# Kernel tuning notes

Hardware: AMD Instinct MI355X
Metric: run time of the kernel (lower is better)

Reference implementation:

```python
import jax, jax.numpy as jnp
import numpy as np

B, N_PER, P_PER = 64, 64, 2016   # graphs, nodes/graph, pairs/graph (C(64,2))
IN_DIM, HID, OUT = 64, 128, 10
EDGE_P = 0.125


def _build_graph_structures():
    """Integer preprocessing replicating build_2sets_from_embeddings's
    combinatorics (pairs, iso_type source, triangle-based 2-set edges)."""
    rng = np.random.default_rng(0)
    n, b = N_PER, B
    A = rng.random((b, n, n)) < EDGE_P
    A = np.triu(A, 1)
    A = A | A.transpose(0, 2, 1)                      # symmetric, no self loops
    gs, us, vs = np.nonzero(A)                        # directed edges, both dirs
    edge_index = np.stack([gs * n + us, gs * n + vs]).astype(np.int64)
    batch = np.repeat(np.arange(b), n).astype(np.int64)
    iu, iv = np.triu_indices(n, 1)                    # local pair (u<v) lists
    pidx = np.full((n, n), -1, np.int64)
    pidx[iu, iv] = np.arange(P_PER)
    pidx[iv, iu] = np.arange(P_PER)                   # symmetric lookup = sorted()
    pair_u = (np.arange(b)[:, None] * n + iu[None, :]).ravel().astype(np.int64)
    pair_v = (np.arange(b)[:, None] * n + iv[None, :]).ravel().astype(np.int64)
    iso_type = A[:, iu, iv].astype(np.float32).ravel()[:, None]  # [B*P_PER,1]
    # 2-set edges: pair (u,v) -> sorted(v,w) and sorted(u,w) for every common
    # neighbor w of u and v (matches _build_2set_edges exactly)
    common = A[:, iu, :] & A[:, iv, :]                # (B, P_PER, n)
    g2, ps, ws = np.nonzero(common)
    u, v = iu[ps], iv[ps]
    d1 = pidx[v, ws]
    d2 = pidx[u, ws]
    src = np.concatenate([g2 * P_PER + ps, g2 * P_PER + ps])
    dst = np.concatenate([g2 * P_PER + d1, g2 * P_PER + d2])
    two_edges = np.stack([src, dst]).astype(np.int64)
    two_batch = np.repeat(np.arange(b), P_PER).astype(np.int64)
    return edge_index, batch, pair_u, pair_v, iso_type, two_edges, two_batch


def setup_inputs() -> dict:
    ei, batch, pu, pv, iso, te, tb = _build_graph_structures()
    key = jax.random.key(0)
    ks = jax.random.split(key, 16)
    w = lambda k, i, o: jax.random.normal(k, (i, o), jnp.float32) / np.float32(np.sqrt(i))
    two_in = 2 * HID + 1
    return {
        "x": jax.random.normal(ks[0], (B * N_PER, IN_DIM), jnp.float32),
        "g1_W1_0": w(ks[1], IN_DIM, HID), "g1_W2_0": w(ks[2], IN_DIM, HID),
        "g1_W1_1": w(ks[3], HID, HID),    "g1_W2_1": w(ks[4], HID, HID),
        "g1_W1_2": w(ks[5], HID, HID),    "g1_W2_2": w(ks[6], HID, HID),
        "k_W1_0": w(ks[7], two_in, HID),  "k_W2_0": w(ks[8], two_in, HID),
        "k_W1_1": w(ks[9], HID, HID),     "k_W2_1": w(ks[10], HID, HID),
        "c_W0": w(ks[11], 2 * HID, HID),  "c_b0": jnp.zeros((HID,), jnp.float32),
        "c_W1": w(ks[12], HID, OUT),      "c_b1": jnp.zeros((OUT,), jnp.float32),
        "iso_type": jnp.asarray(iso),
        "edge_index": jnp.asarray(ei), "batch": jnp.asarray(batch),
        "pair_u": jnp.asarray(pu), "pair_v": jnp.asarray(pv),
        "two_edges": jnp.asarray(te), "two_batch": jnp.asarray(tb),
    }


def _mp_layer(h, ei, W1, W2):
    # relu( h @ W1 + scatter_add_{dst}( h[src] @ W2 ) )  -- OneGNNLayer / KSetLayer
    msg = h[ei[0]] @ W2
    agg = jax.ops.segment_sum(msg, ei[1], num_segments=h.shape[0])
    return jax.nn.relu(h @ W1 + agg)


def reference(x, g1_W1_0, g1_W2_0, g1_W1_1, g1_W2_1, g1_W1_2, g1_W2_2,
              k_W1_0, k_W2_0, k_W1_1, k_W2_1,
              c_W0, c_b0, c_W1, c_b1,
              iso_type, edge_index, batch, pair_u, pair_v, two_edges, two_batch):
    h = _mp_layer(x, edge_index, g1_W1_0, g1_W2_0)
    h = _mp_layer(h, edge_index, g1_W1_1, g1_W2_1)
    h = _mp_layer(h, edge_index, g1_W1_2, g1_W2_2)
    graph_emb_1 = jax.ops.segment_sum(h, batch, num_segments=B)
    # 2-set features: [h_u, h_v, iso_type]  -> [P, 2H+1]
    two_x = jnp.concatenate([h[pair_u], h[pair_v], iso_type], axis=1)
    h2 = _mp_layer(two_x, two_edges, k_W1_0, k_W2_0)
    h2 = _mp_layer(h2, two_edges, k_W1_1, k_W2_1)
    graph_emb_2 = jax.ops.segment_sum(h2, two_batch, num_segments=B)
    combined = jnp.concatenate([graph_emb_1, graph_emb_2], axis=1)
    hc = jax.nn.relu(combined @ c_W0 + c_b0)   # Dropout(p=0.5) inactive in eval
    return hc @ c_W1 + c_b1
```

## Files before the change

kernel.cpp:

```cpp
#include <hip/hip_runtime.h>
#include <hip/hip_bf16.h>


typedef short s16x8 __attribute__((ext_vector_type(8)));
typedef float f32x4 __attribute__((ext_vector_type(4)));

__device__ __forceinline__ unsigned short f2bf(float f) {
  union { float f; unsigned u; } x; x.f = f;
  unsigned r = (x.u + 0x7fffu + ((x.u >> 16) & 1u)) >> 16;
  return (unsigned short)r;
}
__device__ __forceinline__ float bf2f(unsigned short h) {
  union { unsigned u; float f; } x; x.u = ((unsigned)h) << 16;
  return x.f;
}
__device__ __forceinline__ float4 ldbf4(const unsigned short* p) {
  ushort4 q = *(const ushort4*)p;
  return make_float4(bf2f(q.x), bf2f(q.y), bf2f(q.z), bf2f(q.w));
}
__device__ __forceinline__ void stbf4(unsigned short* p, float4 v) {
  ushort4 q;
  q.x = f2bf(v.x); q.y = f2bf(v.y); q.z = f2bf(v.z); q.w = f2bf(v.w);
  *(ushort4*)p = q;
}
__device__ __forceinline__ float4 ld4(const float* p) { return *(const float4*)p; }

template<int KCS, int ASTR>
__device__ __forceinline__ void mfma_dual_lds(
    const unsigned short* A, const unsigned short* Wfrag,
    f32x4 (&accA)[8], f32x4 (&accB)[8])
{
  const int lane = threadIdx.x & 63;
  const int wv = threadIdx.x >> 6;
  const int row = wv * 16 + (lane & 15);
  const int k0 = (lane >> 4) << 3;
  const unsigned short* ap = A + row * ASTR + k0;
  const unsigned short* wp = Wfrag + (size_t)lane * 8;
#pragma unroll
  for (int i = 0; i < 8; ++i) { accA[i] = (f32x4)0.f; accB[i] = (f32x4)0.f; }
#pragma unroll
  for (int kc = 0; kc < KCS; ++kc) {
    s16x8 af = *(const s16x8*)(ap + kc * 32);
#pragma unroll
    for (int nt = 0; nt < 8; ++nt) {
      s16x8 b0 = *(const s16x8*)(wp + ((size_t)((nt)*KCS + kc) << 9));
      s16x8 b1 = *(const s16x8*)(wp + ((size_t)((8 + nt) * KCS + kc) << 9));
      accA[nt] = __builtin_amdgcn_mfma_f32_16x16x32_bf16(af, b0, accA[nt], 0, 0, 0);
      accB[nt] = __builtin_amdgcn_mfma_f32_16x16x32_bf16(af, b1, accB[nt], 0, 0, 0);
    }
  }
}

template<int KCS, int ASTR>
__device__ __forceinline__ void mfma_dual_lds16(
    const unsigned short* A, const unsigned short* Wfrag,
    f32x4 (&accA)[2], f32x4 (&accB)[2])
{
  const int lane = threadIdx.x & 63;
  const int w16 = threadIdx.x >> 6;
  const int rw = w16 & 3, ch = w16 >> 2;
  const int row = rw * 16 + (lane & 15);
  const int k0 = (lane >> 4) << 3;
  const unsigned short* ap = A + row * ASTR + k0;
  const unsigned short* wp = Wfrag + (size_t)lane * 8;
  accA[0] = (f32x4)0.f; accA[1] = (f32x4)0.f;
  accB[0] = (f32x4)0.f; accB[1] = (f32x4)0.f;
  __builtin_amdgcn_s_setprio(1);
#pragma unroll
  for (int kc = 0; kc < KCS; ++kc) {
    s16x8 af = *(const s16x8*)(ap + kc * 32);
#pragma unroll
    for (int n2 = 0; n2 < 2; ++n2) {
      int nt = ch * 2 + n2;
      s16x8 b0 = *(const s16x8*)(wp + ((size_t)(nt * KCS + kc) << 9));
      s16x8 b1 = *(const s16x8*)(wp + ((size_t)((8 + nt) * KCS + kc) << 9));
      accA[n2] = __builtin_amdgcn_mfma_f32_16x16x32_bf16(af, b0, accA[n2], 0, 0, 0);
      accB[n2] = __builtin_amdgcn_mfma_f32_16x16x32_bf16(af, b1, accB[n2], 0, 0, 0);
    }
  }
  __builtin_amdgcn_s_setprio(0);
}

__device__ __forceinline__ void epi_lds16(const f32x4 (&accA)[2], const f32x4 (&accB)[2],
    unsigned short (*preS)[136], unsigned short (*msgS)[136])
{
  const int lane = threadIdx.x & 63;
  const int w16 = threadIdx.x >> 6;
  const int rw = w16 & 3, ch = w16 >> 2;
  const int col = lane & 15;
  const int r0 = rw * 16 + ((lane >> 4) << 2);
  __syncthreads();
#pragma unroll
  for (int n2 = 0; n2 < 2; ++n2) {
    int nt = ch * 2 + n2;
#pragma unroll
    for (int r = 0; r < 4; ++r) {
      preS[r0 + r][nt * 16 + col] = f2bf(accA[n2][r]);
      msgS[r0 + r][nt * 16 + col] = f2bf(accB[n2][r]);
    }
  }
  __syncthreads();
}

__device__ __forceinline__ void epi_global(const f32x4 (&accA)[8], const f32x4 (&accB)[8],
    unsigned short (*sOut)[136], unsigned short* Ca, unsigned short* Cb, long tile)
{
  const int tid = threadIdx.x;
  const int lane = tid & 63;
  const int wv = tid >> 6;
  const int col = lane & 15;
  const int r0 = wv * 16 + ((lane >> 4) << 2);
  const long rowBase = tile * 64;
#pragma unroll
  for (int sel = 0; sel < 2; ++sel) {
    __syncthreads();
#pragma unroll
    for (int nt = 0; nt < 8; ++nt) {
#pragma unroll
      for (int r = 0; r < 4; ++r)
        sOut[r0 + r][nt * 16 + col] = f2bf(sel ? accB[nt][r] : accA[nt][r]);
    }
    __syncthreads();
    unsigned short* C = sel ? Cb : Ca;
#pragma unroll
    for (int i = 0; i < 4; ++i) {
      int fi = tid + i * 256;
      int row = fi >> 4;
      int c8 = fi & 15;
      *(uint4*)(C + (rowBase + row) * 128 + c8 * 8) = *(uint4*)&sOut[row][c8 * 8];
    }
  }
}

struct NArgs {
  const float* x;
  const int* ei;
  const int* gstart;
  const unsigned short *Wf0, *Wf1, *Wf2;
  unsigned short* Hn;
  float* ge1;
  int E1;
};

__global__ __launch_bounds__(1024) void node_stage(NArgs a)
{
  __shared__ __align__(16) unsigned short hS[64][136];
  __shared__ __align__(16) unsigned short preS[64][136];
  __shared__ __align__(16) unsigned short msgS[64][136];
  __shared__ int ldeg[64], lcur[64], loff[65];
  __shared__ unsigned short ledge[1024];
  __shared__ float sge[128];

  const int b = blockIdx.x;
  const int t = threadIdx.x;
  const int base = b * 64;

  const int es = a.gstart[b], ee = a.gstart[b + 1];
  if (t < 64) ldeg[t] = 0;
  if (t < 128) sge[t] = 0.f;
  __syncthreads();
  for (int i = es + t; i < ee; i += 1024)
    atomicAdd(&ldeg[a.ei[a.E1 + i] - base], 1);
  __syncthreads();
  if (t < 64) {
    int v = ldeg[t], s = v;
#pragma unroll
    for (int d = 1; d < 64; d <<= 1) {
      int o = __shfl_up(s, d, 64);
      if (t >= d) s += o;
    }
    loff[t] = s - v;
    lcur[t] = s - v;
    if (t == 63) loff[64] = s;
  }
  unsigned short* xs = &preS[0][0];
  for (int i = t; i < 64 * 64; i += 1024) {
    int r = i >> 6, c = i & 63;
    xs[r * 72 + c] = f2bf(a.x[(size_t)(base + r) * 64 + c]);
  }
  __syncthreads();
  for (int i = es + t; i < ee; i += 1024) {
    int s = a.ei[i] - base, d = a.ei[a.E1 + i] - base;
    int pos = atomicAdd(&lcur[d], 1);
    ledge[pos] = (unsigned short)s;
  }
  __syncthreads();

  f32x4 accA[2], accB[2];
  const int grp = t >> 5, f = (t & 31) * 4;

  mfma_dual_lds16<2, 72>(xs, a.Wf0, accA, accB);
  epi_lds16(accA, accB, preS, msgS);
  for (int r = grp; r < 64; r += 32) {
    float4 acc = ldbf4(&preS[r][f]);
    int j1 = loff[r + 1];
    for (int j = loff[r]; j < j1; ++j) {
      float4 m = ldbf4(&msgS[ledge[j]][f]);
      acc.x += m.x; acc.y += m.y; acc.z += m.z; acc.w += m.w;
    }
    stbf4(&hS[r][f], make_float4(fmaxf(acc.x, 0.f), fmaxf(acc.y, 0.f),
                                 fmaxf(acc.z, 0.f), fmaxf(acc.w, 0.f)));
  }
  __syncthreads();

  mfma_dual_lds16<4, 136>(&hS[0][0], a.Wf1, accA, accB);
  epi_lds16(accA, accB, preS, msgS);
  for (int r = grp; r < 64; r += 32) {
    float4 acc = ldbf4(&preS[r][f]);
    int j1 = loff[r + 1];
    for (int j = loff[r]; j < j1; ++j) {
      float4 m = ldbf4(&msgS[ledge[j]][f]);
      acc.x += m.x; acc.y += m.y; acc.z += m.z; acc.w += m.w;
    }
    stbf4(&hS[r][f], make_float4(fmaxf(acc.x, 0.f), fmaxf(acc.y, 0.f),
                                 fmaxf(acc.z, 0.f), fmaxf(acc.w, 0.f)));
  }
  __syncthreads();

  mfma_dual_lds16<4, 136>(&hS[0][0], a.Wf2, accA, accB);
  epi_lds16(accA, accB, preS, msgS);
  {
    float4 g = make_float4(0.f, 0.f, 0.f, 0.f);
    for (int r = grp; r < 64; r += 32) {
      float4 acc = ldbf4(&preS[r][f]);
      int j1 = loff[r + 1];
      for (int j = loff[r]; j < j1; ++j) {
        float4 m = ldbf4(&msgS[ledge[j]][f]);
        acc.x += m.x; acc.y += m.y; acc.z += m.z; acc.w += m.w;
      }
      float4 o = make_float4(fmaxf(acc.x, 0.f), fmaxf(acc.y, 0.f),
                             fmaxf(acc.z, 0.f), fmaxf(acc.w, 0.f));
      stbf4(&hS[r][f], o);
      g.x += o.x; g.y += o.y; g.z += o.z; g.w += o.w;
    }
    atomicAdd(&sge[f + 0], g.x);
    atomicAdd(&sge[f + 1], g.y);
    atomicAdd(&sge[f + 2], g.z);
    atomicAdd(&sge[f + 3], g.w);
  }
  __syncthreads();
  if (t < 128) a.ge1[b * 128 + t] = sge[t];
  {
    int row = t >> 4, c8 = t & 15;
    *(uint4*)(a.Hn + (size_t)(base + row) * 128 + c8 * 8) = *(uint4*)&hS[row][c8 * 8];
  }
}

__global__ __launch_bounds__(256) void hv_gemm(
    const unsigned short* __restrict__ Hn,
    const unsigned short* __restrict__ Wf3, const unsigned short* __restrict__ Wf4,
    unsigned short* __restrict__ HU1, unsigned short* __restrict__ HU2,
    unsigned short* __restrict__ HV1, unsigned short* __restrict__ HV2)
{
  __shared__ __align__(16) unsigned short hS[64][136];
  const int g = blockIdx.x >> 1;
  const int sel = blockIdx.x & 1;
  const int tid = threadIdx.x;
  const unsigned short* src = Hn + (size_t)g * 64 * 128;
#pragma unroll
  for (int i = 0; i < 4; ++i) {
    int fi = tid + i * 256;
    int row = fi >> 4, c8 = fi & 15;
    *(uint4*)&hS[row][c8 * 8] = *(const uint4*)(src + row * 128 + c8 * 8);
  }
  __syncthreads();
  f32x4 accA[8], accB[8];
  mfma_dual_lds<4, 136>(&hS[0][0], sel ? Wf4 : Wf3, accA, accB);
  epi_global(accA, accB, hS, sel ? HV1 : HU1, sel ? HV2 : HU2, g);
}

struct PrepArgs {
  const float* wa[6];
  const float* wb[6];
  unsigned short* Wf[6];
  const int* te; int E2;
  int* degP;
  const int* ei; int E1;
  int* gstart;
  int nCnt;
};

__global__ void prep(PrepArgs p)
{
  int bb = blockIdx.x, t = threadIdx.x;
  if (bb < 88) {
    int gid = bb * 256 + t;
    if (gid < 22528) {
      int pi, local, kcs, kclog;
      if (gid < 2048) { pi = 0; local = gid; kcs = 2; kclog = 1; }
      else { int r = gid - 2048; pi = 1 + (r >> 12); local = r & 4095; kcs = 4; kclog = 2; }
      int lane = local & 63;
      int t1 = local >> 6;
      int kc = t1 & (kcs - 1);
      int t2 = t1 >> kclog;
      int nt = t2 & 7;
      int wsel = t2 >> 3;
      const float* W = wsel ? p.wb[pi] : p.wa[pi];
      int k0 = kc * 32 + ((lane >> 4) << 3);
      int n = nt * 16 + (lane & 15);
      unsigned short tmp[8];
#pragma unroll
      for (int j = 0; j < 8; ++j) tmp[j] = f2bf(W[(size_t)(k0 + j) * 128 + n]);
      *(uint4*)(p.Wf[pi] + (size_t)local * 8) = *(uint4*)tmp;
    }
  } else if (bb < 88 + p.nCnt) {
    int e = (bb - 88) * 256 + t;
    if (e < p.E2) atomicAdd(&p.degP[p.te[p.E2 + e]], 1);
  } else {
    int e = (bb - 88 - p.nCnt) * 256 + t;
    if (e <= p.E1) {
      int ge = (e < p.E1) ? (p.ei[e] >> 6) : 64;
      int gp = (e > 0) ? (p.ei[e - 1] >> 6) : -1;
      for (int g = gp + 1; g <= ge; ++g) p.gstart[g] = e;
    }
  }
}

__global__ __launch_bounds__(256) void scan_reduce(const int* __restrict__ deg,
                                                   int* __restrict__ bsum, int n)
{
  __shared__ int s[256];
  int b = blockIdx.x, t = threadIdx.x;
  int base = b * 1024;
  int v = 0;
#pragma unroll
  for (int i = 0; i < 4; ++i) {
    int idx = base + t + i * 256;
    if (idx < n) v += deg[idx];
  }
  s[t] = v;
  __syncthreads();
  for (int d = 128; d > 0; d >>= 1) {
    if (t < d) s[t] += s[t + d];
    __syncthreads();
  }
  if (t == 0) bsum[b] = s[0];
}

__global__ __launch_bounds__(256) void scan_final(const int* __restrict__ deg,
                                                  const int* __restrict__ bsum,
                                                  int* __restrict__ off,
                                                  int* __restrict__ cur, int n, int nb)
{
  __shared__ int s[256];
  __shared__ int basePfx;
  int b = blockIdx.x, t = threadIdx.x;
  if (t == 0) {
    int acc = 0;
    for (int k = 0; k < b; ++k) acc += bsum[k];
    basePfx = acc;
  }
  int base = b * 1024 + t * 4;
  int v0 = 0, v1 = 0, v2 = 0, v3 = 0;
  if (base + 0 < n) v0 = deg[base + 0];
  if (base + 1 < n) v1 = deg[base + 1];
  if (base + 2 < n) v2 = deg[base + 2];
  if (base + 3 < n) v3 = deg[base + 3];
  s[t] = v0 + v1 + v2 + v3;
  __syncthreads();
  for (int d = 1; d < 256; d <<= 1) {
    int v = (t >= d) ? s[t - d] : 0;
    __syncthreads();
    s[t] += v;
    __syncthreads();
  }
  int run = basePfx + ((t == 0) ? 0 : s[t - 1]);
  if (base + 0 < n) { off[base + 0] = run; cur[base + 0] = run; run += v0; }
  if (base + 1 < n) { off[base + 1] = run; cur[base + 1] = run; run += v1; }
  if (base + 2 < n) { off[base + 2] = run; cur[base + 2] = run; run += v2; }
  if (base + 3 < n) { off[base + 3] = run; cur[base + 3] = run; run += v3; }
  if (b == nb - 1 && t == 0) off[n] = basePfx + bsum[b];
}

__global__ void csr_fill_pair(const int* __restrict__ te, int E2,
                              const int* __restrict__ pu, const int* __restrict__ pv,
                              const float* __restrict__ iso,
                              int* __restrict__ curP, int4* __restrict__ recP)
{
  int e = blockIdx.x * 256 + threadIdx.x;
  if (e >= E2) return;
  int s = te[e], d = te[E2 + e];
  int pos = atomicAdd(&curP[d], 1);
  recP[pos] = make_int4(pu[s], pv[s], __float_as_int(iso[s]), s);
}

__global__ __launch_bounds__(256) void gather_two0_bf(
    const unsigned short* __restrict__ HU1, const unsigned short* __restrict__ HV1,
    const unsigned short* __restrict__ HU2, const unsigned short* __restrict__ HV2,
    const float* __restrict__ iso,
    const float* __restrict__ w1iso, const float* __restrict__ w2iso,
    const int* __restrict__ pu, const int* __restrict__ pv,
    const int* __restrict__ off, const int4* __restrict__ rec,
    unsigned short* __restrict__ out, int P)
{
  int blk = (int)blockIdx.x;
  const int nB = (int)gridDim.x;
  if ((nB & 7) == 0)
    blk = (blk & 7) * (nB >> 3) + (blk >> 3);
  int p = blk * 8 + (threadIdx.x >> 5);
  if (p >= P) return;
  int f = (threadIdx.x & 31) * 4;
  float4 wi1 = ld4(w1iso + f);
  float4 wi2 = ld4(w2iso + f);
  int u0 = pu[p], v0 = pv[p];
  float is0 = iso[p];
  float4 a = ldbf4(HU1 + (size_t)u0 * 128 + f);
  float4 b = ldbf4(HV1 + (size_t)v0 * 128 + f);
  float4 acc;
  acc.x = a.x + b.x + is0 * wi1.x;
  acc.y = a.y + b.y + is0 * wi1.y;
  acc.z = a.z + b.z + is0 * wi1.z;
  acc.w = a.w + b.w + is0 * wi1.w;
  int j = off[p], e1 = off[p + 1];
  for (; j + 1 < e1; j += 2) {
    int4 r0 = rec[j], r1 = rec[j + 1];
    float4 mu0 = ldbf4(HU2 + (size_t)r0.x * 128 + f);
    float4 mv0 = ldbf4(HV2 + (size_t)r0.y * 128 + f);
    float4 mu1 = ldbf4(HU2 + (size_t)r1.x * 128 + f);
    float4 mv1 = ldbf4(HV2 + (size_t)r1.y * 128 + f);
    float i0 = __int_as_float(r0.z), i1 = __int_as_float(r1.z);
    acc.x += mu0.x + mv0.x + i0 * wi2.x + mu1.x + mv1.x + i1 * wi2.x;
    acc.y += mu0.y + mv0.y + i0 * wi2.y + mu1.y + mv1.y + i1 * wi2.y;
    acc.z += mu0.z + mv0.z + i0 * wi2.z + mu1.z + mv1.z + i1 * wi2.z;
    acc.w += mu0.w + mv0.w + i0 * wi2.w + mu1.w + mv1.w + i1 * wi2.w;
  }
  if (j < e1) {
    int4 r0 = rec[j];
    float4 mu0 = ldbf4(HU2 + (size_t)r0.x * 128 + f);
    float4 mv0 = ldbf4(HV2 + (size_t)r0.y * 128 + f);
    float i0 = __int_as_float(r0.z);
    acc.x += mu0.x + mv0.x + i0 * wi2.x;
    acc.y += mu0.y + mv0.y + i0 * wi2.y;
    acc.z += mu0.z + mv0.z + i0 * wi2.z;
    acc.w += mu0.w + mv0.w + i0 * wi2.w;
  }
  stbf4(out + (size_t)p * 128 + f,
        make_float4(fmaxf(acc.x, 0.f), fmaxf(acc.y, 0.f),
                    fmaxf(acc.z, 0.f), fmaxf(acc.w, 0.f)));
}

__global__ __launch_bounds__(64) void pair_l1(
    const unsigned short* __restrict__ H2,
    const unsigned short* __restrict__ Wfrag,
    const int* __restrict__ off, const int4* __restrict__ rec,
    float* __restrict__ gep)
{
  __shared__ __align__(16) unsigned short hS[16][136];
  __shared__ int offS[17];
  __shared__ int recwS[256];
  __shared__ float sge[128];

  const int tid = threadIdx.x;
  int qt = (int)blockIdx.x;
  const int nB = (int)gridDim.x;
  if ((nB & 7) == 0)
    qt = (qt & 7) * (nB >> 3) + (qt >> 3);
  const int r0 = qt * 16;

  if (tid < 17) offS[tid] = off[r0 + tid];
  sge[tid] = 0.f;
  sge[tid + 64] = 0.f;

  {
    const unsigned short* src = H2 + (size_t)r0 * 128;
#pragma unroll
    for (int i = 0; i < 4; ++i) {
      int fi = tid + i * 64;
      int row = fi >> 4, c8 = fi & 15;
      *(uint4*)&hS[row][c8 * 8] = *(const uint4*)(src + row * 128 + c8 * 8);
    }
  }
  __syncthreads();

  const int e0 = offS[0];
  const int ecnt = offS[16] - e0;
  const bool useS = (ecnt <= 256);
  if (useS)
    for (int j = tid; j < ecnt; j += 64) recwS[j] = rec[e0 + j].w;

  const int lane = tid;
  const int arow = lane & 15;
  const int k0 = (lane >> 4) << 3;
  const unsigned short* hp = &hS[0][0] + arow * 136 + k0;
  const unsigned short* wp = Wfrag + (size_t)lane * 8;
  f32x4 acc[8];
#pragma unroll
  for (int nt = 0; nt < 8; ++nt) acc[nt] = (f32x4)0.f;
  __builtin_amdgcn_s_setprio(1);
#pragma unroll
  for (int kc = 0; kc < 4; ++kc) {
    s16x8 ah = *(const s16x8*)(hp + kc * 32);
#pragma unroll
    for (int nt = 0; nt < 8; ++nt) {
      s16x8 b0 = *(const s16x8*)(wp + ((size_t)(nt * 4 + kc) << 9));
      acc[nt] = __builtin_amdgcn_mfma_f32_16x16x32_bf16(ah, b0, acc[nt], 0, 0, 0);
    }
  }
  __builtin_amdgcn_s_setprio(0);
  __syncthreads();

  {
    const int grp = tid >> 5, f = (tid & 31) * 4;
    for (int i = grp; i < 16; i += 2) {
      float4 a = make_float4(0.f, 0.f, 0.f, 0.f);
      int j = offS[i], e1 = offS[i + 1];
      for (; j + 1 < e1; j += 2) {
        int s0 = useS ? recwS[j - e0] : rec[j].w;
        int s1 = useS ? recwS[j + 1 - e0] : rec[j + 1].w;
        float4 m0 = ldbf4(H2 + (size_t)s0 * 128 + f);
        float4 m1 = ldbf4(H2 + (size_t)s1 * 128 + f);
        a.x += m0.x + m1.x; a.y += m0.y + m1.y;
        a.z += m0.z + m1.z; a.w += m0.w + m1.w;
      }
      if (j < e1) {
        int s0 = useS ? recwS[j - e0] : rec[j].w;
        float4 m0 = ldbf4(H2 + (size_t)s0 * 128 + f);
        a.x += m0.x; a.y += m0.y; a.z += m0.z; a.w += m0.w;
      }
      stbf4(&hS[i][f], a);
    }
  }
  __syncthreads();

  __builtin_amdgcn_s_setprio(1);
#pragma unroll
  for (int kc = 0; kc < 4; ++kc) {
    s16x8 ag = *(const s16x8*)(hp + kc * 32);
#pragma unroll
    for (int nt = 0; nt < 8; ++nt) {
      s16x8 b1 = *(const s16x8*)(wp + ((size_t)((8 + nt) * 4 + kc) << 9));
      acc[nt] = __builtin_amdgcn_mfma_f32_16x16x32_bf16(ag, b1, acc[nt], 0, 0, 0);
    }
  }
  __builtin_amdgcn_s_setprio(0);

  const int col0 = lane & 15;
#pragma unroll
  for (int nt = 0; nt < 8; ++nt) {
    float s = fmaxf(acc[nt][0], 0.f) + fmaxf(acc[nt][1], 0.f)
            + fmaxf(acc[nt][2], 0.f) + fmaxf(acc[nt][3], 0.f);
    atomicAdd(&sge[nt * 16 + col0], s);
  }
  __syncthreads();
  gep[(size_t)qt * 128 + tid] = sge[tid];
  gep[(size_t)qt * 128 + tid + 64] = sge[tid + 64];
}

__global__ void classifier(const float* __restrict__ ge1, const float* __restrict__ gep,
                           const float* __restrict__ W0, const float* __restrict__ b0,
                           const float* __restrict__ W1, const float* __restrict__ b1,
                           float* __restrict__ out)
{
  __shared__ float comb[256];
  __shared__ float hc[128];
  int g = blockIdx.x, t = threadIdx.x;
  comb[t] = ge1[g * 128 + t];
  float s2 = 0.f;
  const float* gpr = gep + (size_t)g * 126 * 128 + t;
  for (int i = 0; i < 126; ++i) s2 += gpr[i * 128];
  comb[t + 128] = s2;
  __syncthreads();
  float s = b0[t];
  for (int k = 0; k < 256; ++k) s += comb[k] * W0[k * 128 + t];
  hc[t] = fmaxf(s, 0.f);
  __syncthreads();
  if (t < 10) {
    float s2o = b1[t];
    for (int k = 0; k < 128; ++k) s2o += hc[k] * W1[k * 10 + t];
    out[g * 10 + t] = s2o;
  }
}

extern "C" void kernel_launch(void* const* d_in, const int* in_sizes, int n_in,
                              void* d_out, int out_size, void* d_ws, size_t ws_size,
                              hipStream_t stream)
{
  (void)n_in; (void)out_size; (void)ws_size;
  const float* x       = (const float*)d_in[0];
  const float* g1_W1_0 = (const float*)d_in[1];
  const float* g1_W2_0 = (const float*)d_in[2];
  const float* g1_W1_1 = (const float*)d_in[3];
  const float* g1_W2_1 = (const float*)d_in[4];
  const float* g1_W1_2 = (const float*)d_in[5];
  const float* g1_W2_2 = (const float*)d_in[6];
  const float* k_W1_0  = (const float*)d_in[7];
  const float* k_W2_0  = (const float*)d_in[8];
  const float* k_W1_1  = (const float*)d_in[9];
  const float* k_W2_1  = (const float*)d_in[10];
  const float* c_W0    = (const float*)d_in[11];
  const float* c_b0    = (const float*)d_in[12];
  const float* c_W1    = (const float*)d_in[13];
  const float* c_b1    = (const float*)d_in[14];
  const float* iso     = (const float*)d_in[15];
  const int*   ei      = (const int*)d_in[16];
  const int*   pu      = (const int*)d_in[18];
  const int*   pv      = (const int*)d_in[19];
  const int*   te      = (const int*)d_in[20];

  const int N  = in_sizes[0] / 64;
  const int E1 = in_sizes[16] / 2;
  const int P  = in_sizes[18];
  const int E2 = in_sizes[20] / 2;
  const int B  = 64;
  const int nTiles = P / 64;

  const size_t NH = (size_t)N * 128;
  const size_t PH = (size_t)P * 128;

  float* ge1 = (float*)d_ws;
  float* gep = ge1 + 8192;
  unsigned short* HU1 = (unsigned short*)(gep + (size_t)4 * nTiles * 128);
  unsigned short* HV1 = HU1 + NH;
  unsigned short* HU2 = HV1 + NH;
  unsigned short* HV2 = HU2 + NH;
  unsigned short* H2   = HV2 + NH;
  unsigned short* Hn   = H2 + PH;
  unsigned short* Wf0  = Hn + NH;
  unsigned short* Wf1  = Wf0 + 16384;
  unsigned short* Wf2  = Wf1 + 32768;
  unsigned short* Wf3  = Wf2 + 32768;
  unsigned short* Wf4  = Wf3 + 32768;
  unsigned short* Wf5  = Wf4 + 32768;

  size_t ipOff = ((size_t)((char*)(Wf5 + 32768) - (char*)d_ws) + 15) & ~(size_t)15;
  int4* recP   = (int4*)((char*)d_ws + ipOff);
  int* degP    = (int*)(recP + E2);
  int* offP    = degP + P;
  int* curP    = offP + P + 1;
  int* bsumP   = curP + P;
  int* gstartN = bsumP + 128;

  const int nbP  = (P + 1023) / 1024;
  const int nCnt = (E2 + 255) / 256;
  const int nBnd = (E1 + 256) / 256;

  hipMemsetAsync(degP, 0, (size_t)P * 4, stream);

  PrepArgs pa;
  pa.wa[0] = g1_W1_0;           pa.wb[0] = g1_W2_0;
  pa.wa[1] = g1_W1_1;           pa.wb[1] = g1_W2_1;
  pa.wa[2] = g1_W1_2;           pa.wb[2] = g1_W2_2;
  pa.wa[3] = k_W1_0;            pa.wb[3] = k_W2_0;
  pa.wa[4] = k_W1_0 + 128*128;  pa.wb[4] = k_W2_0 + 128*128;
  pa.wa[5] = k_W1_1;            pa.wb[5] = k_W2_1;
  pa.Wf[0] = Wf0; pa.Wf[1] = Wf1; pa.Wf[2] = Wf2;
  pa.Wf[3] = Wf3; pa.Wf[4] = Wf4; pa.Wf[5] = Wf5;
  pa.te = te; pa.E2 = E2; pa.degP = degP;
  pa.ei = ei; pa.E1 = E1; pa.gstart = gstartN; pa.nCnt = nCnt;
  prep<<<88 + nCnt + nBnd, 256, 0, stream>>>(pa);

  scan_reduce<<<nbP, 256, 0, stream>>>(degP, bsumP, P);
  scan_final<<<nbP, 256, 0, stream>>>(degP, bsumP, offP, curP, P, nbP);
  csr_fill_pair<<<nCnt, 256, 0, stream>>>(te, E2, pu, pv, iso, curP, recP);

  NArgs na;
  na.x = x; na.ei = ei; na.gstart = gstartN; na.E1 = E1;
  na.Wf0 = Wf0; na.Wf1 = Wf1; na.Wf2 = Wf2;
  na.Hn = Hn; na.ge1 = ge1;
  node_stage<<<B, 1024, 0, stream>>>(na);

  hv_gemm<<<2 * B, 256, 0, stream>>>(Hn, Wf3, Wf4, HU1, HU2, HV1, HV2);

  gather_two0_bf<<<(P + 7) / 8, 256, 0, stream>>>(HU1, HV1, HU2, HV2, iso,
                                                  k_W1_0 + 256 * 128, k_W2_0 + 256 * 128,
                                                  pu, pv, offP, recP, H2, P);

  pair_l1<<<nTiles * 4, 64, 0, stream>>>(H2, Wf5, offP, recP, gep);

  classifier<<<B, 128, 0, stream>>>(ge1, gep, c_W0, c_b0, c_W1, c_b1, (float*)d_out);
}
```

Measured before the change: 284.6 us.

## Fold pair-degree scan kernels into node and hv GEMM launches as extra blocks

The two-pass prefix scan over pair degrees now runs inside existing kernels instead of as standalone launches. The block-sum reduction becomes extra 1024-thread blocks of the node stage, and the final scan becomes extra blocks of the hv GEMM kernel. This removes two kernel launches and lets scan work overlap with the per-graph compute. In exchange, node_plus declares an extra 4 KB shared array that every block allocates, which could lower occupancy, and the scan blocks compete with compute blocks for CUs.

```diff
diff --git a/kernel.cpp b/kernel.cpp
--- a/kernel.cpp
+++ b/kernel.cpp
@@ -140,9 +140,12 @@
   unsigned short* Hn;
   float* ge1;
   int E1;
+  const int* degP;
+  int* bsumP;
+  int P;
 };
 
-__global__ __launch_bounds__(1024) void node_stage(NArgs a)
+__global__ __launch_bounds__(1024) void node_plus(NArgs a)
 {
   __shared__ __align__(16) unsigned short hS[64][136];
   __shared__ __align__(16) unsigned short preS[64][136];
@@ -150,9 +153,24 @@
   __shared__ int ldeg[64], lcur[64], loff[65];
   __shared__ unsigned short ledge[1024];
   __shared__ float sge[128];
+  __shared__ int rs[1024];
+
+  const int t = threadIdx.x;
+
+  if ((int)blockIdx.x >= 64) {
+    int chunk = blockIdx.x - 64;
+    int idx = chunk * 1024 + t;
+    rs[t] = (idx < a.P) ? a.degP[idx] : 0;
+    __syncthreads();
+    for (int d = 512; d > 0; d >>= 1) {
+      if (t < d) rs[t] += rs[t + d];
+      __syncthreads();
+    }
+    if (t == 0) a.bsumP[chunk] = rs[0];
+    return;
+  }
 
   const int b = blockIdx.x;
-  const int t = threadIdx.x;
   const int base = b * 64;
 
   const int es = a.gstart[b], ee = a.gstart[b + 1];
@@ -246,17 +264,57 @@
   }
 }
 
-__global__ __launch_bounds__(256) void hv_gemm(
-    const unsigned short* __restrict__ Hn,
-    const unsigned short* __restrict__ Wf3, const unsigned short* __restrict__ Wf4,
-    unsigned short* __restrict__ HU1, unsigned short* __restrict__ HU2,
-    unsigned short* __restrict__ HV1, unsigned short* __restrict__ HV2)
+struct HArgs {
+  const unsigned short* Hn;
+  const unsigned short *Wf3, *Wf4;
+  unsigned short *HU1, *HU2, *HV1, *HV2;
+  const int* degP;
+  const int* bsumP;
+  int* offP; int* curP;
+  int P; int nb;
+};
+
+__global__ __launch_bounds__(256) void hv_plus(HArgs a)
 {
   __shared__ __align__(16) unsigned short hS[64][136];
+  __shared__ int s[256];
+  __shared__ int basePfx;
+  const int tid = threadIdx.x;
+
+  if ((int)blockIdx.x >= 128) {
+    int b = blockIdx.x - 128;
+    int t = tid;
+    if (t == 0) {
+      int acc = 0;
+      for (int k = 0; k < b; ++k) acc += a.bsumP[k];
+      basePfx = acc;
+    }
+    int base = b * 1024 + t * 4;
+    int v0 = 0, v1 = 0, v2 = 0, v3 = 0;
+    if (base + 0 < a.P) v0 = a.degP[base + 0];
+    if (base + 1 < a.P) v1 = a.degP[base + 1];
+    if (base + 2 < a.P) v2 = a.degP[base + 2];
+    if (base + 3 < a.P) v3 = a.degP[base + 3];
+    s[t] = v0 + v1 + v2 + v3;
+    __syncthreads();
+    for (int d = 1; d < 256; d <<= 1) {
+      int v = (t >= d) ? s[t - d] : 0;
+      __syncthreads();
+      s[t] += v;
+      __syncthreads();
+    }
+    int run = basePfx + ((t == 0) ? 0 : s[t - 1]);
+    if (base + 0 < a.P) { a.offP[base + 0] = run; a.curP[base + 0] = run; run += v0; }
+    if (base + 1 < a.P) { a.offP[base + 1] = run; a.curP[base + 1] = run; run += v1; }
+    if (base + 2 < a.P) { a.offP[base + 2] = run; a.curP[base + 2] = run; run += v2; }
+    if (base + 3 < a.P) { a.offP[base + 3] = run; a.curP[base + 3] = run; run += v3; }
+    if (b == a.nb - 1 && t == 0) a.offP[a.P] = basePfx + a.bsumP[b];
+    return;
+  }
+
   const int g = blockIdx.x >> 1;
   const int sel = blockIdx.x & 1;
-  const int tid = threadIdx.x;
-  const unsigned short* src = Hn + (size_t)g * 64 * 128;
+  const unsigned short* src = a.Hn + (size_t)g * 64 * 128;
 #pragma unroll
   for (int i = 0; i < 4; ++i) {
     int fi = tid + i * 256;
@@ -265,8 +323,8 @@
   }
   __syncthreads();
   f32x4 accA[8], accB[8];
-  mfma_dual_lds<4, 136>(&hS[0][0], sel ? Wf4 : Wf3, accA, accB);
-  epi_global(accA, accB, hS, sel ? HV1 : HU1, sel ? HV2 : HU2, g);
+  mfma_dual_lds<4, 136>(&hS[0][0], sel ? a.Wf4 : a.Wf3, accA, accB);
+  epi_global(accA, accB, hS, sel ? a.HV1 : a.HU1, sel ? a.HV2 : a.HU2, g);
 }
 
 struct PrepArgs {
@@ -314,62 +372,6 @@
       for (int g = gp + 1; g <= ge; ++g) p.gstart[g] = e;
     }
   }
-}
-
-__global__ __launch_bounds__(256) void scan_reduce(const int* __restrict__ deg,
-                                                   int* __restrict__ bsum, int n)
-{
-  __shared__ int s[256];
-  int b = blockIdx.x, t = threadIdx.x;
-  int base = b * 1024;
-  int v = 0;
-#pragma unroll
-  for (int i = 0; i < 4; ++i) {
-    int idx = base + t + i * 256;
-    if (idx < n) v += deg[idx];
-  }
-  s[t] = v;
-  __syncthreads();
-  for (int d = 128; d > 0; d >>= 1) {
-    if (t < d) s[t] += s[t + d];
-    __syncthreads();
-  }
-  if (t == 0) bsum[b] = s[0];
-}
-
-__global__ __launch_bounds__(256) void scan_final(const int* __restrict__ deg,
-                                                  const int* __restrict__ bsum,
-                                                  int* __restrict__ off,
-                                                  int* __restrict__ cur, int n, int nb)
-{
-  __shared__ int s[256];
-  __shared__ int basePfx;
-  int b = blockIdx.x, t = threadIdx.x;
-  if (t == 0) {
-    int acc = 0;
-    for (int k = 0; k < b; ++k) acc += bsum[k];
-    basePfx = acc;
-  }
-  int base = b * 1024 + t * 4;
-  int v0 = 0, v1 = 0, v2 = 0, v3 = 0;
-  if (base + 0 < n) v0 = deg[base + 0];
-  if (base + 1 < n) v1 = deg[base + 1];
-  if (base + 2 < n) v2 = deg[base + 2];
-  if (base + 3 < n) v3 = deg[base + 3];
-  s[t] = v0 + v1 + v2 + v3;
-  __syncthreads();
-  for (int d = 1; d < 256; d <<= 1) {
-    int v = (t >= d) ? s[t - d] : 0;
-    __syncthreads();
-    s[t] += v;
-    __syncthreads();
-  }
-  int run = basePfx + ((t == 0) ? 0 : s[t - 1]);
-  if (base + 0 < n) { off[base + 0] = run; cur[base + 0] = run; run += v0; }
-  if (base + 1 < n) { off[base + 1] = run; cur[base + 1] = run; run += v1; }
-  if (base + 2 < n) { off[base + 2] = run; cur[base + 2] = run; run += v2; }
-  if (base + 3 < n) { off[base + 3] = run; cur[base + 3] = run; run += v3; }
-  if (b == nb - 1 && t == 0) off[n] = basePfx + bsum[b];
 }
 
 __global__ void csr_fill_pair(const int* __restrict__ te, int E2,
@@ -649,17 +651,21 @@
   pa.ei = ei; pa.E1 = E1; pa.gstart = gstartN; pa.nCnt = nCnt;
   prep<<<88 + nCnt + nBnd, 256, 0, stream>>>(pa);
 
-  scan_reduce<<<nbP, 256, 0, stream>>>(degP, bsumP, P);
-  scan_final<<<nbP, 256, 0, stream>>>(degP, bsumP, offP, curP, P, nbP);
-  csr_fill_pair<<<nCnt, 256, 0, stream>>>(te, E2, pu, pv, iso, curP, recP);
-
   NArgs na;
   na.x = x; na.ei = ei; na.gstart = gstartN; na.E1 = E1;
   na.Wf0 = Wf0; na.Wf1 = Wf1; na.Wf2 = Wf2;
   na.Hn = Hn; na.ge1 = ge1;
-  node_stage<<<B, 1024, 0, stream>>>(na);
-
-  hv_gemm<<<2 * B, 256, 0, stream>>>(Hn, Wf3, Wf4, HU1, HU2, HV1, HV2);
+  na.degP = degP; na.bsumP = bsumP; na.P = P;
+  node_plus<<<B + nbP, 1024, 0, stream>>>(na);
+
+  HArgs ha;
+  ha.Hn = Hn; ha.Wf3 = Wf3; ha.Wf4 = Wf4;
+  ha.HU1 = HU1; ha.HU2 = HU2; ha.HV1 = HV1; ha.HV2 = HV2;
+  ha.degP = degP; ha.bsumP = bsumP; ha.offP = offP; ha.curP = curP;
+  ha.P = P; ha.nb = nbP;
+  hv_plus<<<2 * B + nbP, 256, 0, stream>>>(ha);
+
+  csr_fill_pair<<<nCnt, 256, 0, stream>>>(te, E2, pu, pv, iso, curP, recP);
 
   gather_two0_bf<<<(P + 7) / 8, 256, 0, stream>>>(HU1, HV1, HU2, HV2, iso,
                                                   k_W1_0 + 256 * 128, k_W2_0 + 256 * 128,
```

Result: faster. 268.7 us, median of 2 (-5.6%).
